# Kernel tuning notes

Measured on AMD Instinct MI355X. Metric: run time of the kernel, lower is better.

## Reference

```python
import jax, jax.numpy as jnp
import numpy as np

B, S, DM, H, HD = 2, 2048, 1024, 16, 64
MEM_SIZE = 1000
K_SIMILAR, K_CONTIG = 8, 2
K_TOTAL = K_SIMILAR + K_CONTIG  # 10 memory tokens
NEG = -1e9


def setup_inputs() -> dict:
    key = jax.random.key(0)
    k1, k2, k3, k4, k5, k6 = jax.random.split(key, 6)
    inputs = jax.random.normal(k1, (B, S, DM), dtype=jnp.float32)
    attention_mask = jnp.ones((B, S), dtype=jnp.float32)
    Wq = jax.random.normal(k2, (DM, H * HD), dtype=jnp.float32) * 0.02
    Wk = jax.random.normal(k3, (DM, H * HD), dtype=jnp.float32) * 0.02
    Wv = jax.random.normal(k4, (DM, H * HD), dtype=jnp.float32) * 0.02
    Wo = jax.random.normal(k5, (H * HD, DM), dtype=jnp.float32) * 0.02
    events = jax.random.normal(k6, (MEM_SIZE, H * HD), dtype=jnp.float32) * 0.02
    return {"inputs": inputs, "attention_mask": attention_mask,
            "Wq": Wq, "Wk": Wk, "Wv": Wv, "Wo": Wo, "events": events}


def _forward(inputs, attention_mask, Wq, Wk, Wv, Wo, events):
    # projections (no bias), split heads: [B, H, S, HD]
    q = (inputs @ Wq).reshape(B, S, H, HD).transpose(0, 2, 1, 3)
    k = (inputs @ Wk).reshape(B, S, H, HD).transpose(0, 2, 1, 3)
    v = (inputs @ Wv).reshape(B, S, H, HD).transpose(0, 2, 1, 3)

    # --- episodic retrieval: cosine top-k of last-token key vs events ---
    qvec = k[:, :, -1, :].reshape(B, H * HD)                       # [B, D]
    qn = qvec / (jnp.linalg.norm(qvec, axis=-1, keepdims=True) + 1e-8)
    en = events / (jnp.linalg.norm(events, axis=-1, keepdims=True) + 1e-8)
    sims = qn @ en.T                                               # [B, M]
    _, topk_idx = jax.lax.top_k(sims, K_TOTAL)                     # [B, K]
    retrieved = events[topk_idx]                                   # [B, K, D]
    retrieved_k = retrieved.reshape(B, K_TOTAL, H, HD).transpose(0, 2, 1, 3)  # [B,H,K,HD]
    retrieved_v = retrieved_k                                      # non-differential path

    aug_k = jnp.concatenate([retrieved_k, k], axis=2)              # [B,H,K+S,HD]
    aug_v = jnp.concatenate([retrieved_v, v], axis=2)

    # --- ALiBi bias: slopes * (pos_i - pos_j) on original cols, 0 on memory cols ---
    slopes = 2.0 ** (-8.0 * jnp.arange(1, H + 1, dtype=jnp.float32) / H)  # [H]
    positions = jnp.arange(S, dtype=jnp.float32)
    pos_diff = positions[:, None] - positions[None, :]             # [S, S]
    alibi = slopes[:, None, None] * pos_diff                       # [H, S, S]
    alibi = jnp.concatenate([jnp.zeros((H, S, K_TOTAL), jnp.float32), alibi], axis=-1)

    # --- causal mask: -1e9 strictly-upper on original cols, 0 on memory cols ---
    tri = jnp.where(jnp.arange(S)[None, :] > jnp.arange(S)[:, None], NEG, 0.0)  # [S,S]
    causal = jnp.concatenate([jnp.zeros((S, K_TOTAL), jnp.float32), tri], axis=-1)

    # --- padding mask: memory tokens always attendable ---
    aug_mask = jnp.concatenate([jnp.ones((B, K_TOTAL), jnp.float32), attention_mask], axis=-1)
    mask_bias = (1.0 - aug_mask)[:, None, None, :] * NEG           # [B,1,1,K+S]

    scores = jnp.einsum("bhqd,bhkd->bhqk", q, aug_k) / np.sqrt(HD)
    scores = scores + alibi[None] + causal[None, None] + mask_bias
    attn = jax.nn.softmax(scores, axis=-1)
    out = jnp.einsum("bhqk,bhkd->bhqd", attn, aug_v)               # [B,H,S,HD]
    out = out.transpose(0, 2, 1, 3).reshape(B, S, H * HD)
    return out @ Wo


def reference(inputs, attention_mask, Wq, Wk, Wv, Wo, events):
    return _forward(inputs, attention_mask, Wq, Wk, Wv, Wo, events)
```

## Files before the change

### kernel.cpp

```cpp
#include <hip/hip_runtime.h>
#include <hip/hip_bf16.h>
#include <math.h>

#define B_   2
#define S_   2048
#define DM_  1024
#define H_   16
#define HD_  64
#define MEM_ 1000
#define KTOT 10
#define NROW (B_ * S_)
#define NEG9 (-1e9f)
#define LDK  72
#define QITEMS 128
#define SC_  0.18033688f
#define TH_  170.238f

typedef __attribute__((ext_vector_type(8))) short short8;
typedef __attribute__((ext_vector_type(4))) float f32x4;

__device__ __forceinline__ float __exp2(float x) { return __builtin_amdgcn_exp2f(x); }

__device__ __forceinline__ void gll16(const __hip_bfloat16* g, __hip_bfloat16* l) {
    __builtin_amdgcn_global_load_lds(
        (const __attribute__((address_space(1))) void*)g,
        (__attribute__((address_space(3))) void*)l, 16, 0, 0);
}

__global__ __launch_bounds__(256) void prep(const float* __restrict__ inputs,
                                            const float* __restrict__ Wq,
                                            const float* __restrict__ Wk,
                                            const float* __restrict__ Wv,
                                            const float* __restrict__ Wo,
                                            __hip_bfloat16* __restrict__ Ax,
                                            __hip_bfloat16* __restrict__ Wt,
                                            float* __restrict__ lk,
                                            int* __restrict__ ctr) {
    const int bx = blockIdx.x, tid = threadIdx.x;
    if (bx == 0 && tid < 8) ctr[tid] = 0;

    if (bx < 2048) {
        const size_t i = ((size_t)bx * 256 + tid) * 8;
        float4 a = *(const float4*)&inputs[i];
        float4 b = *(const float4*)&inputs[i + 4];
        alignas(16) __hip_bfloat16 t[8];
        t[0] = __float2bfloat16(a.x); t[1] = __float2bfloat16(a.y);
        t[2] = __float2bfloat16(a.z); t[3] = __float2bfloat16(a.w);
        t[4] = __float2bfloat16(b.x); t[5] = __float2bfloat16(b.y);
        t[6] = __float2bfloat16(b.z); t[7] = __float2bfloat16(b.w);
        *(short8*)&Ax[i] = *(short8*)t;
        return;
    }
    if (bx < 3072) {
        const int idx = bx - 2048;
        const int g = idx >> 8, rem = idx & 255;
        const float* W = (g == 0) ? Wq : (g == 1) ? Wk : (g == 2) ? Wv : Wo;
        const int n0 = (rem & 15) * 64, k0 = (rem >> 4) * 64;
        __shared__ float T[64][65];
        {
            const int r = tid >> 4, c4 = (tid & 15) * 4;
#pragma unroll
            for (int p = 0; p < 4; ++p) {
                float4 v = *(const float4*)&W[(size_t)(k0 + r + p * 16) * 1024 + n0 + c4];
                T[r + p * 16][c4 + 0] = v.x; T[r + p * 16][c4 + 1] = v.y;
                T[r + p * 16][c4 + 2] = v.z; T[r + p * 16][c4 + 3] = v.w;
            }
        }
        __syncthreads();
        {
            const int n = tid >> 3, off = (tid & 7) * 8;
#pragma unroll
            for (int p = 0; p < 2; ++p) {
                const int nn = n + p * 32;
                alignas(16) __hip_bfloat16 t[8];
#pragma unroll
                for (int j = 0; j < 8; ++j) t[j] = __float2bfloat16(T[off + j][nn]);
                *(short8*)&Wt[((size_t)(g * 1024 + n0 + nn)) * 1024 + k0 + off] = *(short8*)t;
            }
        }
        return;
    }
    {
        const int idx = bx - 3072;
        const int xblk = idx & 15, b = idx >> 4;
        const int cl = tid & 63;
        const int col = xblk * 64 + cl;
        const int kq = tid >> 6;
        __shared__ float xr[1024];
        __shared__ float part[4][64];
        for (int i = tid; i < 1024; i += 256)
            xr[i] = inputs[((size_t)(b * S_ + S_ - 1)) * 1024 + i];
        __syncthreads();
        float acc = 0.f;
#pragma unroll 4
        for (int k = kq * 256; k < kq * 256 + 256; ++k)
            acc += xr[k] * Wk[(size_t)k * 1024 + col];
        part[kq][cl] = acc;
        __syncthreads();
        if (tid < 64)
            lk[b * 1024 + xblk * 64 + tid] =
                part[0][tid] + part[1][tid] + part[2][tid] + part[3][tid];
    }
}

__device__ __forceinline__ void store_out(__hip_bfloat16* p, float x) { *p = __float2bfloat16(x); }
__device__ __forceinline__ void store_out(float* p, float x) { *p = x; }

template <typename OutT>
__global__ __launch_bounds__(256) void gemm_mfma(const __hip_bfloat16* __restrict__ A,
                                                 const __hip_bfloat16* __restrict__ Bt,
                                                 OutT* __restrict__ C, int ldc) {
    __shared__ __hip_bfloat16 As[128 * 32];
    __shared__ __hip_bfloat16 Bs[128 * 32];
    const int tid = threadIdx.x;
    const int wave = tid >> 6, lane = tid & 63;
    const int quad = lane >> 4, lm = lane & 15;
    const int wr = wave >> 1, wc = wave & 1;
    const int m0 = blockIdx.y * 128, n0 = blockIdx.x * 128;

    const int r0 = tid >> 2, c0 = (tid & 3) * 8;
    const __hip_bfloat16* ga0 = &A[(size_t)(m0 + r0) * 1024 + c0];
    const __hip_bfloat16* ga1 = &A[(size_t)(m0 + 64 + r0) * 1024 + c0];
    const __hip_bfloat16* gb0 = &Bt[(size_t)(n0 + r0) * 1024 + c0];
    const __hip_bfloat16* gb1 = &Bt[(size_t)(n0 + 64 + r0) * 1024 + c0];
    __hip_bfloat16* la0 = &As[(wave * 64) * 8];
    __hip_bfloat16* la1 = &As[(256 + wave * 64) * 8];
    __hip_bfloat16* lb0 = &Bs[(wave * 64) * 8];
    __hip_bfloat16* lb1 = &Bs[(256 + wave * 64) * 8];

    f32x4 acc[4][4];
#pragma unroll
    for (int i = 0; i < 4; ++i)
#pragma unroll
        for (int j = 0; j < 4; ++j) acc[i][j] = (f32x4){0.f, 0.f, 0.f, 0.f};

    for (int k0 = 0; k0 < 1024; k0 += 32) {
        __syncthreads();
        gll16(ga0 + k0, la0);
        gll16(ga1 + k0, la1);
        gll16(gb0 + k0, lb0);
        gll16(gb1 + k0, lb1);
        __syncthreads();
        short8 af[4], bf4[4];
#pragma unroll
        for (int mt = 0; mt < 4; ++mt)
            af[mt] = *(const short8*)&As[(wr * 64 + mt * 16 + lm) * 32 + quad * 8];
#pragma unroll
        for (int nt = 0; nt < 4; ++nt)
            bf4[nt] = *(const short8*)&Bs[(wc * 64 + nt * 16 + lm) * 32 + quad * 8];
#pragma unroll
        for (int mt = 0; mt < 4; ++mt)
#pragma unroll
            for (int nt = 0; nt < 4; ++nt)
                acc[mt][nt] = __builtin_amdgcn_mfma_f32_16x16x32_bf16(
                    af[mt], bf4[nt], acc[mt][nt], 0, 0, 0);
    }
#pragma unroll
    for (int mt = 0; mt < 4; ++mt)
#pragma unroll
        for (int nt = 0; nt < 4; ++nt) {
            const int col = n0 + wc * 64 + nt * 16 + lm;
#pragma unroll
            for (int i = 0; i < 4; ++i) {
                const int row = m0 + wr * 64 + mt * 16 + quad * 4 + i;
                store_out(&C[(size_t)row * ldc + col], acc[mt][nt][i]);
            }
        }
}

template <typename OutT>
__global__ __launch_bounds__(256) void gemm_mfma64(const __hip_bfloat16* __restrict__ A,
                                                   const __hip_bfloat16* __restrict__ Bt,
                                                   OutT* __restrict__ C, int ldc) {
    __shared__ __hip_bfloat16 As[64 * 32];
    __shared__ __hip_bfloat16 Bs[128 * 32];
    const int tid = threadIdx.x;
    const int wave = tid >> 6, lane = tid & 63;
    const int quad = lane >> 4, lm = lane & 15;
    const int wr = wave >> 1, wc = wave & 1;
    const int m0 = blockIdx.y * 64, n0 = blockIdx.x * 128;

    const int r0 = tid >> 2, c0 = (tid & 3) * 8;
    const __hip_bfloat16* ga  = &A[(size_t)(m0 + r0) * 1024 + c0];
    const __hip_bfloat16* gb0 = &Bt[(size_t)(n0 + r0) * 1024 + c0];
    const __hip_bfloat16* gb1 = &Bt[(size_t)(n0 + 64 + r0) * 1024 + c0];
    __hip_bfloat16* la  = &As[(wave * 64) * 8];
    __hip_bfloat16* lb0 = &Bs[(wave * 64) * 8];
    __hip_bfloat16* lb1 = &Bs[(256 + wave * 64) * 8];

    f32x4 acc[2][4];
#pragma unroll
    for (int i = 0; i < 2; ++i)
#pragma unroll
        for (int j = 0; j < 4; ++j) acc[i][j] = (f32x4){0.f, 0.f, 0.f, 0.f};

    for (int k0 = 0; k0 < 1024; k0 += 32) {
        __syncthreads();
        gll16(ga + k0, la);
        gll16(gb0 + k0, lb0);
        gll16(gb1 + k0, lb1);
        __syncthreads();
        short8 af[2], bf4[4];
#pragma unroll
        for (int mt = 0; mt < 2; ++mt)
            af[mt] = *(const short8*)&As[(wr * 32 + mt * 16 + lm) * 32 + quad * 8];
#pragma unroll
        for (int nt = 0; nt < 4; ++nt)
            bf4[nt] = *(const short8*)&Bs[(wc * 64 + nt * 16 + lm) * 32 + quad * 8];
#pragma unroll
        for (int mt = 0; mt < 2; ++mt)
#pragma unroll
            for (int nt = 0; nt < 4; ++nt)
                acc[mt][nt] = __builtin_amdgcn_mfma_f32_16x16x32_bf16(
                    af[mt], bf4[nt], acc[mt][nt], 0, 0, 0);
    }
#pragma unroll
    for (int mt = 0; mt < 2; ++mt)
#pragma unroll
        for (int nt = 0; nt < 4; ++nt) {
            const int col = n0 + wc * 64 + nt * 16 + lm;
#pragma unroll
            for (int i = 0; i < 4; ++i) {
                const int row = m0 + wr * 32 + mt * 16 + quad * 4 + i;
                store_out(&C[(size_t)row * ldc + col], acc[mt][nt][i]);
            }
        }
}

__global__ __launch_bounds__(256) void sims_kernel(const float* __restrict__ lk,
                                                   const float* __restrict__ events,
                                                   float* __restrict__ sims) {
    const int b = blockIdx.y;
    const int tid = threadIdx.x;
    const int wave = tid >> 6, lane = tid & 63;
    __shared__ float qv[1024];
    for (int i = tid; i < 1024; i += 256)
        qv[i] = lk[b * 1024 + i];
    __syncthreads();

    const int m = blockIdx.x * 4 + wave;
    if (m >= MEM_) return;
    const float* ev = &events[(size_t)m * 1024];
    float dot = 0.f, nrm = 0.f;
    for (int d = lane; d < 1024; d += 64) {
        float e = ev[d];
        dot += qv[d] * e;
        nrm += e * e;
    }
    for (int off = 32; off; off >>= 1) {
        dot += __shfl_down(dot, off);
        nrm += __shfl_down(nrm, off);
    }
    if (lane == 0) sims[b * 1024 + m] = dot / (sqrtf(nrm) + 1e-8f);
}

__global__ __launch_bounds__(64) void topk10_kernel(const float* __restrict__ sims,
                                                    int* __restrict__ topk) {
    const int b = blockIdx.x;
    const int lane = threadIdx.x;
    const int base = lane * 16;
    float v[16];
#pragma unroll
    for (int j = 0; j < 16; ++j) {
        const int m = base + j;
        v[j] = (m < MEM_) ? sims[b * 1024 + m] : -INFINITY;
    }
    for (int it = 0; it < KTOT; ++it) {
        float best = -INFINITY; int bi = 0x7fffffff;
#pragma unroll
        for (int j = 0; j < 16; ++j)
            if (v[j] > best) { best = v[j]; bi = base + j; }
        for (int off = 32; off; off >>= 1) {
            const float ob = __shfl_xor(best, off);
            const int   oi = __shfl_xor(bi, off);
            if (ob > best || (ob == best && oi < bi)) { best = ob; bi = oi; }
        }
        if (lane == 0) topk[b * KTOT + it] = bi;
#pragma unroll
        for (int j = 0; j < 16; ++j)
            if (base + j == bi) v[j] = -INFINITY;
    }
}

__global__ __launch_bounds__(256) void attn_mfma(
        const __hip_bfloat16* __restrict__ qkv,
        const float* __restrict__ events,
        const int* __restrict__ topk,
        const float* __restrict__ amask,
        __hip_bfloat16* __restrict__ out,
        int* __restrict__ ctr) {
    const int tid = threadIdx.x;
    const int wave = tid >> 6, lane = tid & 63;
    const int quad = lane >> 4, lm = lane & 15;
    const int g = blockIdx.x & 7;

    const __hip_bfloat16* qf = qkv;
    const __hip_bfloat16* kf = qkv + 1024;
    const __hip_bfloat16* vf = qkv + 2048;

    __shared__ __hip_bfloat16 Ks[64 * LDK];
    __shared__ __hip_bfloat16 Vt[80 * LDK];
    __shared__ __hip_bfloat16 Ps[64 * LDK];
    __shared__ float colb[64];
    __shared__ float redb[4];
    __shared__ int sItem;

    const int va = tid & 31, vdc = tid >> 5;
    const int vtok0 = va * 2, vd0 = vdc * 8;

    for (int i = tid * 8; i < 64 * LDK; i += 256 * 8)
        *(int4*)&Vt[i] = make_int4(0, 0, 0, 0);
    for (int i = tid; i < 16 * LDK; i += 256) {
        const int r = i / LDK;
        Vt[64 * LDK + i] = __float2bfloat16(r == 0 ? 1.0f : 0.0f);
    }

    for (;;) {
        __syncthreads();
        if (tid == 0) sItem = atomicAdd(&ctr[g], 1);
        __syncthreads();
        const int n = sItem;
        if (n >= QITEMS) break;

        const int qt = 31 - (n >> 2);
        const int s  = g * 4 + (n & 3);
        const int h  = 15 - (s >> 1);
        const int b  = s & 1;
        const int q0 = qt * 64;
        const float slope2 = __exp2(-0.5f * (float)(h + 1)) * 1.44269504f;

        short8 pk[2], pv0, pv1;
        float pam = 1.f;
        auto prefetchKV = [&](int kt) {
            const __hip_bfloat16* ks = &kf[((size_t)(b * S_ + kt * 64)) * 3072 + h * 64];
#pragma unroll
            for (int u = 0; u < 2; ++u) {
                int c = tid * 2 + u, row = c >> 3, off = (c & 7) * 8;
                pk[u] = *(const short8*)&ks[(size_t)row * 3072 + off];
            }
            const __hip_bfloat16* v0 =
                &vf[((size_t)(b * S_ + kt * 64 + vtok0)) * 3072 + h * 64 + vd0];
            pv0 = *(const short8*)v0;
            pv1 = *(const short8*)(v0 + 3072);
            if (tid < 64) pam = amask[b * S_ + kt * 64 + tid];
        };
        auto stageKV = [&](int kt) {
#pragma unroll
            for (int u = 0; u < 2; ++u) {
                int c = tid * 2 + u, row = c >> 3, off = (c & 7) * 8;
                *(short8*)&Ks[row * LDK + off] = pk[u];
            }
#pragma unroll
            for (int j = 0; j < 8; ++j) {
                short2 pr; pr.x = pv0[j]; pr.y = pv1[j];
                *(short2*)&Vt[(vd0 + j) * LDK + vtok0] = pr;
            }
            if (tid < 64)
                colb[tid] = fmaf(-slope2, (float)(kt * 64 + tid), (1.f - pam) * NEG9);
        };

        prefetchKV(0);

        short8 qa[2];
        {
            const __hip_bfloat16* qsrc =
                &qf[((size_t)(b * S_ + q0 + wave * 16 + lm)) * 3072 + h * 64 + quad * 8];
            qa[0] = *(const short8*)qsrc;
            qa[1] = *(const short8*)(qsrc + 32);
        }
        if (tid < 80) {
            const int tok = tid >> 3, d0 = (tid & 7) * 8;
            const int ev = topk[b * KTOT + tok];
            const float* es = &events[(size_t)ev * 1024 + h * 64 + d0];
#pragma unroll
            for (int j = 0; j < 8; ++j) {
                __hip_bfloat16 x = __float2bfloat16(es[j]);
                Ks[tok * LDK + d0 + j] = x;
                Vt[(d0 + j) * LDK + tok] = x;
            }
        }

        float m_[4], mshift[4];
        f32x4 Oa[5];
#pragma unroll
        for (int i = 0; i < 4; ++i) {
            m_[i] = -INFINITY;
            mshift[i] = -slope2 * (float)(q0 + wave * 16 + quad * 4 + i);
        }
#pragma unroll
        for (int nt = 0; nt < 5; ++nt) Oa[nt] = (f32x4){0.f, 0.f, 0.f, 0.f};

        auto qk = [&](f32x4* sa) {
#pragma unroll
            for (int nt = 0; nt < 4; ++nt) sa[nt] = (f32x4){0.f, 0.f, 0.f, 0.f};
#pragma unroll
            for (int ks2 = 0; ks2 < 2; ++ks2) {
#pragma unroll
                for (int nt = 0; nt < 4; ++nt) {
                    short8 bk = *(const short8*)&Ks[(nt * 16 + lm) * LDK + ks2 * 32 + quad * 8];
                    sa[nt] = __builtin_amdgcn_mfma_f32_16x16x32_bf16(qa[ks2], bk, sa[nt], 0, 0, 0);
                }
            }
        };
        auto pv = [&]() {
#pragma unroll
            for (int ks2 = 0; ks2 < 2; ++ks2) {
                short8 ap = *(const short8*)&Ps[(wave * 16 + lm) * LDK + ks2 * 32 + quad * 8];
#pragma unroll
                for (int nt = 0; nt < 5; ++nt) {
                    short8 bv = *(const short8*)&Vt[(nt * 16 + lm) * LDK + ks2 * 32 + quad * 8];
                    Oa[nt] = __builtin_amdgcn_mfma_f32_16x16x32_bf16(ap, bv, Oa[nt], 0, 0, 0);
                }
            }
        };

        auto softmax_online = [&](const f32x4* sa, int kt, bool diag) {
            float cb[4];
            if (kt >= 0) {
#pragma unroll
                for (int nt = 0; nt < 4; ++nt) cb[nt] = colb[nt * 16 + lm];
            }
#pragma unroll
            for (int i = 0; i < 4; ++i) {
                const int lr = wave * 16 + quad * 4 + i;
                const int rg = q0 + lr;
                float s2[4];
#pragma unroll
                for (int nt = 0; nt < 4; ++nt) {
                    const int cc = nt * 16 + lm;
                    if (kt < 0) {
                        s2[nt] = (cc < KTOT) ? fmaf(sa[nt][i], SC_, mshift[i]) : NEG9;
                    } else {
                        float v = fmaf(sa[nt][i], SC_, cb[nt]);
                        s2[nt] = (diag && kt * 64 + cc > rg) ? NEG9 : v;
                    }
                }
                float rmax = fmaxf(fmaxf(s2[0], s2[1]), fmaxf(s2[2], s2[3]));
#pragma unroll
                for (int off = 1; off < 16; off <<= 1)
                    rmax = fmaxf(rmax, __shfl_xor(rmax, off, 16));
                const float newm = fmaxf(m_[i], rmax);
                const float al = __exp2(m_[i] - newm);
                m_[i] = newm;
#pragma unroll
                for (int nt = 0; nt < 4; ++nt)
                    Ps[lr * LDK + nt * 16 + lm] = __float2bfloat16(__exp2(s2[nt] - newm));
#pragma unroll
                for (int nt = 0; nt < 5; ++nt)
                    Oa[nt][i] *= al;
            }
        };

        auto softmax_fast = [&](const f32x4* sa, int cbase, bool diag) {
            float cb[4];
#pragma unroll
            for (int nt = 0; nt < 4; ++nt) cb[nt] = colb[nt * 16 + lm];
#pragma unroll
            for (int i = 0; i < 4; ++i) {
                const int lr = wave * 16 + quad * 4 + i;
                const float cm = m_[i];
                float p[4];
#pragma unroll
                for (int nt = 0; nt < 4; ++nt)
                    p[nt] = __exp2(fmaf(sa[nt][i], SC_, cb[nt]) - cm);
                if (diag) {
                    const int rg = q0 + lr;
#pragma unroll
                    for (int nt = 0; nt < 4; ++nt)
                        if (cbase + nt * 16 + lm > rg) p[nt] = 0.f;
                }
#pragma unroll
                for (int nt = 0; nt < 4; ++nt)
                    Ps[lr * LDK + nt * 16 + lm] = __float2bfloat16(p[nt]);
            }
        };

        __syncthreads();
        {
            f32x4 sa[4];
            qk(sa);
            softmax_online(sa, -1, false);
            pv();
        }
        __syncthreads();
        stageKV(0);
        __syncthreads();
        if (qt >= 1) prefetchKV(1);
        {
            f32x4 sa[4];
            qk(sa);
            softmax_online(sa, 0, qt == 0);
            pv();
        }

        int ktend = 0;
        if (qt >= 1) {
            float mloc = fminf(fminf(m_[0], m_[1]), fminf(m_[2], m_[3]));
#pragma unroll
            for (int off = 1; off < 64; off <<= 1)
                mloc = fminf(mloc, __shfl_xor(mloc, off, 64));
            if (lane == 0) redb[wave] = mloc;
            __syncthreads();
            const float mmin = fminf(fminf(redb[0], redb[1]), fminf(redb[2], redb[3]));
            ktend = min(qt, (int)((TH_ - mmin) / (64.f * slope2)));
        }
        for (int kt = 1; kt <= ktend; ++kt) {
            stageKV(kt);
            __syncthreads();
            if (kt < ktend) prefetchKV(kt + 1);
            f32x4 sa[4];
            qk(sa);
            softmax_fast(sa, kt * 64, kt == qt);
            pv();
            __syncthreads();
        }

#pragma unroll
        for (int i = 0; i < 4; ++i) {
            const int lr = wave * 16 + quad * 4 + i;
            const float l = __shfl(Oa[4][i], (lane & 48));
            const float inv = 1.f / l;
            __hip_bfloat16* dst = &out[((size_t)(b * S_ + q0 + lr)) * 1024 + h * 64 + lm];
#pragma unroll
            for (int nt = 0; nt < 4; ++nt)
                dst[nt * 16] = __float2bfloat16(Oa[nt][i] * inv);
        }
    }
}

extern "C" void kernel_launch(void* const* d_in, const int* in_sizes, int n_in,
                              void* d_out, int out_size, void* d_ws, size_t ws_size,
                              hipStream_t stream) {
    const float* inputs = (const float*)d_in[0];
    const float* amask  = (const float*)d_in[1];
    const float* Wq     = (const float*)d_in[2];
    const float* Wk     = (const float*)d_in[3];
    const float* Wv     = (const float*)d_in[4];
    const float* Wo     = (const float*)d_in[5];
    const float* events = (const float*)d_in[6];
    float* out = (float*)d_out;

    __hip_bfloat16* Ax  = (__hip_bfloat16*)d_ws;
    __hip_bfloat16* Wt  = Ax + (size_t)NROW * 1024;
    __hip_bfloat16* qkv = Wt + (size_t)4096 * 1024;
    __hip_bfloat16* ao  = qkv + (size_t)NROW * 3072;
    float* lk   = (float*)(ao + (size_t)NROW * 1024);
    float* sims = lk + 2 * 1024;
    int* topk   = (int*)(sims + 2 * 1024);
    int* ctr    = topk + B_ * KTOT;

    dim3 blk(256);
    prep<<<3104, blk, 0, stream>>>(inputs, Wq, Wk, Wv, Wo, Ax, Wt, lk, ctr);
    sims_kernel<<<dim3(250, B_), blk, 0, stream>>>(lk, events, sims);
    topk10_kernel<<<B_, 64, 0, stream>>>(sims, topk);
    gemm_mfma<__hip_bfloat16><<<dim3(24, 32), blk, 0, stream>>>(Ax, Wt, qkv, 3072);
    attn_mfma<<<1024, blk, 0, stream>>>(qkv, events, topk, amask, ao, ctr);
    gemm_mfma64<float><<<dim3(8, 64), blk, 0, stream>>>(
        ao, Wt + (size_t)3072 * 1024, out, 1024);
}
```

Baseline: 235.0 us.

## Double attention query tile to 128 rows per block for K/V reuse

Each attention work item now covers 128 query rows instead of 64. Every wave handles two 16-row MFMA tiles and shares each K/V fragment loaded from LDS across both, which halves K/V staging per query and halves the number of work items and blocks. The prefetch of the next K/V tile is also moved ahead of the barrier. In exchange the kernel uses more registers and a larger Ps buffer, has half as many work items for load balance, and applies the diagonal mask over two key tiles.

```diff
diff --git a/kernel.cpp b/kernel.cpp
--- a/kernel.cpp
+++ b/kernel.cpp
@@ -12,7 +12,7 @@
 #define NROW (B_ * S_)
 #define NEG9 (-1e9f)
 #define LDK  72
-#define QITEMS 128
+#define QITEMS 64
 #define SC_  0.18033688f
 #define TH_  170.238f
 
@@ -300,7 +300,7 @@
 
     __shared__ __hip_bfloat16 Ks[64 * LDK];
     __shared__ __hip_bfloat16 Vt[80 * LDK];
-    __shared__ __hip_bfloat16 Ps[64 * LDK];
+    __shared__ __hip_bfloat16 Ps[128 * LDK];
     __shared__ float colb[64];
     __shared__ float redb[4];
     __shared__ int sItem;
@@ -322,11 +322,12 @@
         const int n = sItem;
         if (n >= QITEMS) break;
 
-        const int qt = 31 - (n >> 2);
+        const int qt2 = 15 - (n >> 2);
         const int s  = g * 4 + (n & 3);
         const int h  = 15 - (s >> 1);
         const int b  = s & 1;
-        const int q0 = qt * 64;
+        const int q0 = qt2 * 128;
+        const int qt = 2 * qt2 + 1;
         const float slope2 = __exp2(-0.5f * (float)(h + 1)) * 1.44269504f;
 
         short8 pk[2], pv0, pv1;
@@ -361,12 +362,13 @@
 
         prefetchKV(0);
 
-        short8 qa[2];
-        {
+        short8 qa[2][2];
+#pragma unroll
+        for (int mt = 0; mt < 2; ++mt) {
             const __hip_bfloat16* qsrc =
-                &qf[((size_t)(b * S_ + q0 + wave * 16 + lm)) * 3072 + h * 64 + quad * 8];
-            qa[0] = *(const short8*)qsrc;
-            qa[1] = *(const short8*)(qsrc + 32);
+                &qf[((size_t)(b * S_ + q0 + wave * 32 + mt * 16 + lm)) * 3072 + h * 64 + quad * 8];
+            qa[mt][0] = *(const short8*)qsrc;
+            qa[mt][1] = *(const short8*)(qsrc + 32);
         }
         if (tid < 80) {
             const int tok = tid >> 3, d0 = (tid & 7) * 8;
@@ -380,122 +382,142 @@
             }
         }
 
-        float m_[4], mshift[4];
-        f32x4 Oa[5];
-#pragma unroll
-        for (int i = 0; i < 4; ++i) {
-            m_[i] = -INFINITY;
-            mshift[i] = -slope2 * (float)(q0 + wave * 16 + quad * 4 + i);
-        }
-#pragma unroll
-        for (int nt = 0; nt < 5; ++nt) Oa[nt] = (f32x4){0.f, 0.f, 0.f, 0.f};
-
-        auto qk = [&](f32x4* sa) {
-#pragma unroll
-            for (int nt = 0; nt < 4; ++nt) sa[nt] = (f32x4){0.f, 0.f, 0.f, 0.f};
+        float m_[2][4], mshift[2][4];
+        f32x4 Oa[2][5];
+#pragma unroll
+        for (int mt = 0; mt < 2; ++mt)
+#pragma unroll
+            for (int i = 0; i < 4; ++i) {
+                m_[mt][i] = -INFINITY;
+                mshift[mt][i] = -slope2 * (float)(q0 + wave * 32 + mt * 16 + quad * 4 + i);
+            }
+#pragma unroll
+        for (int mt = 0; mt < 2; ++mt)
+#pragma unroll
+            for (int nt = 0; nt < 5; ++nt) Oa[mt][nt] = (f32x4){0.f, 0.f, 0.f, 0.f};
+
+        auto qk = [&](f32x4 (&sa)[2][4]) {
+#pragma unroll
+            for (int mt = 0; mt < 2; ++mt)
+#pragma unroll
+                for (int nt = 0; nt < 4; ++nt) sa[mt][nt] = (f32x4){0.f, 0.f, 0.f, 0.f};
 #pragma unroll
             for (int ks2 = 0; ks2 < 2; ++ks2) {
 #pragma unroll
                 for (int nt = 0; nt < 4; ++nt) {
                     short8 bk = *(const short8*)&Ks[(nt * 16 + lm) * LDK + ks2 * 32 + quad * 8];
-                    sa[nt] = __builtin_amdgcn_mfma_f32_16x16x32_bf16(qa[ks2], bk, sa[nt], 0, 0, 0);
+#pragma unroll
+                    for (int mt = 0; mt < 2; ++mt)
+                        sa[mt][nt] = __builtin_amdgcn_mfma_f32_16x16x32_bf16(
+                            qa[mt][ks2], bk, sa[mt][nt], 0, 0, 0);
                 }
             }
         };
         auto pv = [&]() {
 #pragma unroll
             for (int ks2 = 0; ks2 < 2; ++ks2) {
-                short8 ap = *(const short8*)&Ps[(wave * 16 + lm) * LDK + ks2 * 32 + quad * 8];
+                short8 ap[2];
+#pragma unroll
+                for (int mt = 0; mt < 2; ++mt)
+                    ap[mt] = *(const short8*)&Ps[(wave * 32 + mt * 16 + lm) * LDK + ks2 * 32 + quad * 8];
 #pragma unroll
                 for (int nt = 0; nt < 5; ++nt) {
                     short8 bv = *(const short8*)&Vt[(nt * 16 + lm) * LDK + ks2 * 32 + quad * 8];
-                    Oa[nt] = __builtin_amdgcn_mfma_f32_16x16x32_bf16(ap, bv, Oa[nt], 0, 0, 0);
+#pragma unroll
+                    for (int mt = 0; mt < 2; ++mt)
+                        Oa[mt][nt] = __builtin_amdgcn_mfma_f32_16x16x32_bf16(
+                            ap[mt], bv, Oa[mt][nt], 0, 0, 0);
                 }
             }
         };
 
-        auto softmax_online = [&](const f32x4* sa, int kt, bool diag) {
+        auto softmax_online = [&](const f32x4 (&sa)[2][4], int kt, bool diag) {
             float cb[4];
             if (kt >= 0) {
 #pragma unroll
                 for (int nt = 0; nt < 4; ++nt) cb[nt] = colb[nt * 16 + lm];
             }
 #pragma unroll
-            for (int i = 0; i < 4; ++i) {
-                const int lr = wave * 16 + quad * 4 + i;
-                const int rg = q0 + lr;
-                float s2[4];
-#pragma unroll
-                for (int nt = 0; nt < 4; ++nt) {
-                    const int cc = nt * 16 + lm;
-                    if (kt < 0) {
-                        s2[nt] = (cc < KTOT) ? fmaf(sa[nt][i], SC_, mshift[i]) : NEG9;
-                    } else {
-                        float v = fmaf(sa[nt][i], SC_, cb[nt]);
-                        s2[nt] = (diag && kt * 64 + cc > rg) ? NEG9 : v;
+            for (int mt = 0; mt < 2; ++mt)
+#pragma unroll
+                for (int i = 0; i < 4; ++i) {
+                    const int lr = wave * 32 + mt * 16 + quad * 4 + i;
+                    const int rg = q0 + lr;
+                    float s2[4];
+#pragma unroll
+                    for (int nt = 0; nt < 4; ++nt) {
+                        const int cc = nt * 16 + lm;
+                        if (kt < 0) {
+                            s2[nt] = (cc < KTOT) ? fmaf(sa[mt][nt][i], SC_, mshift[mt][i]) : NEG9;
+                        } else {
+                            float v = fmaf(sa[mt][nt][i], SC_, cb[nt]);
+                            s2[nt] = (diag && kt * 64 + cc > rg) ? NEG9 : v;
+                        }
                     }
+                    float rmax = fmaxf(fmaxf(s2[0], s2[1]), fmaxf(s2[2], s2[3]));
+#pragma unroll
+                    for (int off = 1; off < 16; off <<= 1)
+                        rmax = fmaxf(rmax, __shfl_xor(rmax, off, 16));
+                    const float newm = fmaxf(m_[mt][i], rmax);
+                    const float al = __exp2(m_[mt][i] - newm);
+                    m_[mt][i] = newm;
+#pragma unroll
+                    for (int nt = 0; nt < 4; ++nt)
+                        Ps[lr * LDK + nt * 16 + lm] = __float2bfloat16(__exp2(s2[nt] - newm));
+#pragma unroll
+                    for (int nt = 0; nt < 5; ++nt)
+                        Oa[mt][nt][i] *= al;
                 }
-                float rmax = fmaxf(fmaxf(s2[0], s2[1]), fmaxf(s2[2], s2[3]));
-#pragma unroll
-                for (int off = 1; off < 16; off <<= 1)
-                    rmax = fmaxf(rmax, __shfl_xor(rmax, off, 16));
-                const float newm = fmaxf(m_[i], rmax);
-                const float al = __exp2(m_[i] - newm);
-                m_[i] = newm;
-#pragma unroll
-                for (int nt = 0; nt < 4; ++nt)
-                    Ps[lr * LDK + nt * 16 + lm] = __float2bfloat16(__exp2(s2[nt] - newm));
-#pragma unroll
-                for (int nt = 0; nt < 5; ++nt)
-                    Oa[nt][i] *= al;
-            }
         };
 
-        auto softmax_fast = [&](const f32x4* sa, int cbase, bool diag) {
+        auto softmax_fast = [&](const f32x4 (&sa)[2][4], int cbase, bool diag) {
             float cb[4];
 #pragma unroll
             for (int nt = 0; nt < 4; ++nt) cb[nt] = colb[nt * 16 + lm];
 #pragma unroll
-            for (int i = 0; i < 4; ++i) {
-                const int lr = wave * 16 + quad * 4 + i;
-                const float cm = m_[i];
-                float p[4];
-#pragma unroll
-                for (int nt = 0; nt < 4; ++nt)
-                    p[nt] = __exp2(fmaf(sa[nt][i], SC_, cb[nt]) - cm);
-                if (diag) {
-                    const int rg = q0 + lr;
+            for (int mt = 0; mt < 2; ++mt)
+#pragma unroll
+                for (int i = 0; i < 4; ++i) {
+                    const int lr = wave * 32 + mt * 16 + quad * 4 + i;
+                    const float cm = m_[mt][i];
+                    float p[4];
 #pragma unroll
                     for (int nt = 0; nt < 4; ++nt)
-                        if (cbase + nt * 16 + lm > rg) p[nt] = 0.f;
+                        p[nt] = __exp2(fmaf(sa[mt][nt][i], SC_, cb[nt]) - cm);
+                    if (diag) {
+                        const int rg = q0 + lr;
+#pragma unroll
+                        for (int nt = 0; nt < 4; ++nt)
+                            if (cbase + nt * 16 + lm > rg) p[nt] = 0.f;
+                    }
+#pragma unroll
+                    for (int nt = 0; nt < 4; ++nt)
+                        Ps[lr * LDK + nt * 16 + lm] = __float2bfloat16(p[nt]);
                 }
-#pragma unroll
-                for (int nt = 0; nt < 4; ++nt)
-                    Ps[lr * LDK + nt * 16 + lm] = __float2bfloat16(p[nt]);
-            }
         };
 
         __syncthreads();
         {
-            f32x4 sa[4];
+            f32x4 sa[2][4];
             qk(sa);
             softmax_online(sa, -1, false);
             pv();
         }
         __syncthreads();
         stageKV(0);
-        __syncthreads();
         if (qt >= 1) prefetchKV(1);
+        __syncthreads();
         {
-            f32x4 sa[4];
+            f32x4 sa[2][4];
             qk(sa);
-            softmax_online(sa, 0, qt == 0);
+            softmax_online(sa, 0, 0 >= qt - 1);
             pv();
         }
 
         int ktend = 0;
-        if (qt >= 1) {
-            float mloc = fminf(fminf(m_[0], m_[1]), fminf(m_[2], m_[3]));
+        {
+            float mloc = fminf(fminf(m_[0][0], m_[0][1]), fminf(m_[0][2], m_[0][3]));
+            mloc = fminf(mloc, fminf(fminf(m_[1][0], m_[1][1]), fminf(m_[1][2], m_[1][3])));
 #pragma unroll
             for (int off = 1; off < 64; off <<= 1)
                 mloc = fminf(mloc, __shfl_xor(mloc, off, 64));
@@ -506,25 +528,28 @@
         }
         for (int kt = 1; kt <= ktend; ++kt) {
             stageKV(kt);
+            if (kt < ktend) prefetchKV(kt + 1);
             __syncthreads();
-            if (kt < ktend) prefetchKV(kt + 1);
-            f32x4 sa[4];
+            f32x4 sa[2][4];
             qk(sa);
-            softmax_fast(sa, kt * 64, kt == qt);
+            softmax_fast(sa, kt * 64, kt >= qt - 1);
             pv();
             __syncthreads();
         }
 
 #pragma unroll
-        for (int i = 0; i < 4; ++i) {
-            const int lr = wave * 16 + quad * 4 + i;
-            const float l = __shfl(Oa[4][i], (lane & 48));
-            const float inv = 1.f / l;
-            __hip_bfloat16* dst = &out[((size_t)(b * S_ + q0 + lr)) * 1024 + h * 64 + lm];
-#pragma unroll
-            for (int nt = 0; nt < 4; ++nt)
-                dst[nt * 16] = __float2bfloat16(Oa[nt][i] * inv);
-        }
+        for (int mt = 0; mt < 2; ++mt)
+#pragma unroll
+            for (int i = 0; i < 4; ++i) {
+                const int lr = wave * 32 + mt * 16 + quad * 4 + i;
+                const float l = __shfl(Oa[mt][4][i], (lane & 48));
+                const float inv = 1.f / l;
+                __hip_bfloat16* dst =
+                    &out[((size_t)(b * S_ + q0 + lr)) * 1024 + h * 64 + lm];
+#pragma unroll
+                for (int nt = 0; nt < 4; ++nt)
+                    dst[nt * 16] = __float2bfloat16(Oa[mt][nt][i] * inv);
+            }
     }
 }
 
@@ -554,7 +579,7 @@
     sims_kernel<<<dim3(250, B_), blk, 0, stream>>>(lk, events, sims);
     topk10_kernel<<<B_, 64, 0, stream>>>(sims, topk);
     gemm_mfma<__hip_bfloat16><<<dim3(24, 32), blk, 0, stream>>>(Ax, Wt, qkv, 3072);
-    attn_mfma<<<1024, blk, 0, stream>>>(qkv, events, topk, amask, ao, ctr);
+    attn_mfma<<<512, blk, 0, stream>>>(qkv, events, topk, amask, ao, ctr);
     gemm_mfma64<float><<<dim3(8, 64), blk, 0, stream>>>(
         ao, Wt + (size_t)3072 * 1024, out, 1024);
 }
```

Result: no change. 231.6 us (-1.5%).

## Transpose QK^T MFMA so each lane owns a query row; vectorize P stores

Applied to the files above, without the earlier changes.

Swaps the MFMA operands so the score tile comes out transposed: each lane holds one query row, and its 4 accumulator entries are consecutive key columns. Row max then needs only two cross-quad shuffles instead of a 4-step butterfly per row, and column biases load as float4. P values are written as packed 4-element bf16 stores instead of scalar stores. The alpha rescale now needs per-row shuffles, and the barriers are reordered so the prefetch is issued before the sync that separates staging from compute.

```diff
diff --git a/kernel.cpp b/kernel.cpp
--- a/kernel.cpp
+++ b/kernel.cpp
@@ -17,6 +17,7 @@
 #define TH_  170.238f
 
 typedef __attribute__((ext_vector_type(8))) short short8;
+typedef __attribute__((ext_vector_type(4))) short s16x4;
 typedef __attribute__((ext_vector_type(4))) float f32x4;
 
 __device__ __forceinline__ float __exp2(float x) { return __builtin_amdgcn_exp2f(x); }
@@ -329,6 +330,9 @@
         const int q0 = qt * 64;
         const float slope2 = __exp2(-0.5f * (float)(h + 1)) * 1.44269504f;
 
+        const int rg = q0 + wave * 16 + lm;
+        const float mshift = -slope2 * (float)rg;
+
         short8 pk[2], pv0, pv1;
         float pam = 1.f;
         auto prefetchKV = [&](int kt) {
@@ -380,13 +384,8 @@
             }
         }
 
-        float m_[4], mshift[4];
+        float m_ = -INFINITY;
         f32x4 Oa[5];
-#pragma unroll
-        for (int i = 0; i < 4; ++i) {
-            m_[i] = -INFINITY;
-            mshift[i] = -slope2 * (float)(q0 + wave * 16 + quad * 4 + i);
-        }
 #pragma unroll
         for (int nt = 0; nt < 5; ++nt) Oa[nt] = (f32x4){0.f, 0.f, 0.f, 0.f};
 
@@ -398,7 +397,7 @@
 #pragma unroll
                 for (int nt = 0; nt < 4; ++nt) {
                     short8 bk = *(const short8*)&Ks[(nt * 16 + lm) * LDK + ks2 * 32 + quad * 8];
-                    sa[nt] = __builtin_amdgcn_mfma_f32_16x16x32_bf16(qa[ks2], bk, sa[nt], 0, 0, 0);
+                    sa[nt] = __builtin_amdgcn_mfma_f32_16x16x32_bf16(bk, qa[ks2], sa[nt], 0, 0, 0);
                 }
             }
         };
@@ -415,63 +414,69 @@
         };
 
         auto softmax_online = [&](const f32x4* sa, int kt, bool diag) {
-            float cb[4];
-            if (kt >= 0) {
-#pragma unroll
-                for (int nt = 0; nt < 4; ++nt) cb[nt] = colb[nt * 16 + lm];
-            }
-#pragma unroll
-            for (int i = 0; i < 4; ++i) {
-                const int lr = wave * 16 + quad * 4 + i;
-                const int rg = q0 + lr;
-                float s2[4];
+            float s2[4][4];
+            if (kt < 0) {
+#pragma unroll
+                for (int nt = 0; nt < 4; ++nt)
+#pragma unroll
+                    for (int i = 0; i < 4; ++i) {
+                        const int kl = nt * 16 + quad * 4 + i;
+                        s2[nt][i] = (kl < KTOT) ? fmaf(sa[nt][i], SC_, mshift) : NEG9;
+                    }
+            } else {
 #pragma unroll
                 for (int nt = 0; nt < 4; ++nt) {
-                    const int cc = nt * 16 + lm;
-                    if (kt < 0) {
-                        s2[nt] = (cc < KTOT) ? fmaf(sa[nt][i], SC_, mshift[i]) : NEG9;
-                    } else {
-                        float v = fmaf(sa[nt][i], SC_, cb[nt]);
-                        s2[nt] = (diag && kt * 64 + cc > rg) ? NEG9 : v;
+                    const float4 c4 = *(const float4*)&colb[nt * 16 + quad * 4];
+                    const float cc[4] = {c4.x, c4.y, c4.z, c4.w};
+#pragma unroll
+                    for (int i = 0; i < 4; ++i) {
+                        float v = fmaf(sa[nt][i], SC_, cc[i]);
+                        if (diag && kt * 64 + nt * 16 + quad * 4 + i > rg) v = NEG9;
+                        s2[nt][i] = v;
                     }
                 }
-                float rmax = fmaxf(fmaxf(s2[0], s2[1]), fmaxf(s2[2], s2[3]));
-#pragma unroll
-                for (int off = 1; off < 16; off <<= 1)
-                    rmax = fmaxf(rmax, __shfl_xor(rmax, off, 16));
-                const float newm = fmaxf(m_[i], rmax);
-                const float al = __exp2(m_[i] - newm);
-                m_[i] = newm;
-#pragma unroll
-                for (int nt = 0; nt < 4; ++nt)
-                    Ps[lr * LDK + nt * 16 + lm] = __float2bfloat16(__exp2(s2[nt] - newm));
-#pragma unroll
-                for (int nt = 0; nt < 5; ++nt)
-                    Oa[nt][i] *= al;
-            }
+            }
+            float rmax = s2[0][0];
+#pragma unroll
+            for (int nt = 0; nt < 4; ++nt)
+#pragma unroll
+                for (int i = 0; i < 4; ++i) rmax = fmaxf(rmax, s2[nt][i]);
+            rmax = fmaxf(rmax, __shfl_xor(rmax, 16));
+            rmax = fmaxf(rmax, __shfl_xor(rmax, 32));
+            const float newm = fmaxf(m_, rmax);
+            const float al = __exp2(m_ - newm);
+            m_ = newm;
+#pragma unroll
+            for (int nt = 0; nt < 4; ++nt) {
+                alignas(8) __hip_bfloat16 w[4];
+#pragma unroll
+                for (int i = 0; i < 4; ++i)
+                    w[i] = __float2bfloat16(__exp2(s2[nt][i] - newm));
+                *(s16x4*)&Ps[(wave * 16 + lm) * LDK + nt * 16 + quad * 4] = *(s16x4*)w;
+            }
+            float alq[4];
+#pragma unroll
+            for (int i = 0; i < 4; ++i) alq[i] = __shfl(al, quad * 4 + i);
+#pragma unroll
+            for (int nt = 0; nt < 5; ++nt)
+#pragma unroll
+                for (int i = 0; i < 4; ++i) Oa[nt][i] *= alq[i];
         };
 
         auto softmax_fast = [&](const f32x4* sa, int cbase, bool diag) {
-            float cb[4];
-#pragma unroll
-            for (int nt = 0; nt < 4; ++nt) cb[nt] = colb[nt * 16 + lm];
-#pragma unroll
-            for (int i = 0; i < 4; ++i) {
-                const int lr = wave * 16 + quad * 4 + i;
-                const float cm = m_[i];
-                float p[4];
-#pragma unroll
-                for (int nt = 0; nt < 4; ++nt)
-                    p[nt] = __exp2(fmaf(sa[nt][i], SC_, cb[nt]) - cm);
-                if (diag) {
-                    const int rg = q0 + lr;
-#pragma unroll
-                    for (int nt = 0; nt < 4; ++nt)
-                        if (cbase + nt * 16 + lm > rg) p[nt] = 0.f;
+            const float cm = m_;
+#pragma unroll
+            for (int nt = 0; nt < 4; ++nt) {
+                const float4 c4 = *(const float4*)&colb[nt * 16 + quad * 4];
+                const float cc[4] = {c4.x, c4.y, c4.z, c4.w};
+                alignas(8) __hip_bfloat16 w[4];
+#pragma unroll
+                for (int i = 0; i < 4; ++i) {
+                    float p = __exp2(fmaf(sa[nt][i], SC_, cc[i]) - cm);
+                    if (diag && cbase + nt * 16 + quad * 4 + i > rg) p = 0.f;
+                    w[i] = __float2bfloat16(p);
                 }
-#pragma unroll
-                for (int nt = 0; nt < 4; ++nt)
-                    Ps[lr * LDK + nt * 16 + lm] = __float2bfloat16(p[nt]);
+                *(s16x4*)&Ps[(wave * 16 + lm) * LDK + nt * 16 + quad * 4] = *(s16x4*)w;
             }
         };
 
@@ -484,8 +489,8 @@
         }
         __syncthreads();
         stageKV(0);
-        __syncthreads();
         if (qt >= 1) prefetchKV(1);
+        __syncthreads();
         {
             f32x4 sa[4];
             qk(sa);
@@ -495,7 +500,7 @@
 
         int ktend = 0;
         if (qt >= 1) {
-            float mloc = fminf(fminf(m_[0], m_[1]), fminf(m_[2], m_[3]));
+            float mloc = m_;
 #pragma unroll
             for (int off = 1; off < 64; off <<= 1)
                 mloc = fminf(mloc, __shfl_xor(mloc, off, 64));
@@ -505,14 +510,14 @@
             ktend = min(qt, (int)((TH_ - mmin) / (64.f * slope2)));
         }
         for (int kt = 1; kt <= ktend; ++kt) {
+            __syncthreads();
             stageKV(kt);
+            if (kt < ktend) prefetchKV(kt + 1);
             __syncthreads();
-            if (kt < ktend) prefetchKV(kt + 1);
             f32x4 sa[4];
             qk(sa);
             softmax_fast(sa, kt * 64, kt == qt);
             pv();
-            __syncthreads();
         }
 
 #pragma unroll
```

Measured after the change: 235.7 us. Within noise of the previous version (+0.3%).
